# Performance work log

Measured on AMD Instinct MI355X. Metric: run time of the kernel, lower is better.

The kernel has to match this reference:

```python
import jax, jax.numpy as jnp
import numpy as np

N_HEAD = 16

def setup_inputs() -> dict:
    key = jax.random.key(0)
    k1, k2, k3 = jax.random.split(key, 3)
    B, T, C = 2, 2048, 1024
    x = jax.random.normal(k1, (B, T, C), dtype=jnp.float32)
    W_attn = jax.random.normal(k2, (C, 3 * C), dtype=jnp.float32) * (C ** -0.5)
    b_attn = jnp.zeros((3 * C,), dtype=jnp.float32)
    W_proj = jax.random.normal(k3, (C, C), dtype=jnp.float32) * (C ** -0.5)
    b_proj = jnp.zeros((C,), dtype=jnp.float32)
    return {"x": x, "W_attn": W_attn, "b_attn": b_attn, "W_proj": W_proj, "b_proj": b_proj}

def reference(x, W_attn, b_attn, W_proj, b_proj):
    B, T, C = x.shape
    H = N_HEAD
    D = C // H  # head_dim
    scale = D ** -0.5
    qkv = x @ W_attn + b_attn                       # [B,T,3C]
    q, k, v = jnp.split(qkv, 3, axis=-1)
    # [B,T,C] -> [B,H,T,D]
    q = q.reshape(B, T, H, D).transpose(0, 2, 1, 3)
    k = k.reshape(B, T, H, D).transpose(0, 2, 1, 3)
    v = v.reshape(B, T, H, D).transpose(0, 2, 1, 3)
    att = jnp.einsum('bhqd,bhkd->bhqk', q, k) * scale
    causal = jnp.tril(jnp.ones((T, T), dtype=bool))
    att = jnp.where(causal, att, jnp.float32(-jnp.inf))
    att = jax.nn.softmax(att, axis=-1)
    y = jnp.einsum('bhqk,bhkd->bhqd', att, v)       # [B,H,T,D]
    y = y.transpose(0, 2, 1, 3).reshape(B, T, C)
    return y @ W_proj + b_proj
```

## Files before the change

### kernel.cpp

```cpp
#include <hip/hip_runtime.h>

typedef __bf16 bf16;
typedef __bf16 bf16x4 __attribute__((ext_vector_type(4)));
typedef __bf16 bf16x8 __attribute__((ext_vector_type(8)));
typedef short s16x4 __attribute__((ext_vector_type(4)));
typedef float f32x4 __attribute__((ext_vector_type(4)));
typedef unsigned int u32x4 __attribute__((ext_vector_type(4)));

#define NB 2
#define NT 2048
#define NC 1024
#define NH 16
#define ND 64

#if __has_builtin(__builtin_amdgcn_exp2f)
#define EXP2F(x) __builtin_amdgcn_exp2f(x)
#else
#define EXP2F(x) __expf(0.69314718055994531f * (x))
#endif

#if __has_builtin(__builtin_amdgcn_rcpf)
#define RCPF(x) __builtin_amdgcn_rcpf(x)
#else
#define RCPF(x) (1.0f / (x))
#endif

__device__ __forceinline__ void async16(const void* g, void* l) {
  __builtin_amdgcn_global_load_lds(
      (const __attribute__((address_space(1))) void*)g,
      (__attribute__((address_space(3))) void*)l, 16, 0, 0);
}

__device__ __forceinline__ bf16x8 ld8(const bf16* p) {
  return *reinterpret_cast<const bf16x8*>(p);
}
__device__ __forceinline__ bf16x4 ld4(const bf16* p) {
  return *reinterpret_cast<const bf16x4*>(p);
}

__device__ __forceinline__ f32x4 mfma16(bf16x4 a, bf16x4 b, f32x4 c) {
  s16x4 ai = __builtin_bit_cast(s16x4, a);
  s16x4 bi = __builtin_bit_cast(s16x4, b);
#if __has_builtin(__builtin_amdgcn_mfma_f32_16x16x16bf16_1k)
  return __builtin_amdgcn_mfma_f32_16x16x16bf16_1k(ai, bi, c, 0, 0, 0);
#else
  f32x4 d;
  asm("v_mfma_f32_16x16x16_bf16 %0, %1, %2, %3"
      : "=v"(d) : "v"(ai), "v"(bi), "v"(c));
  return d;
#endif
}

__global__ __launch_bounds__(256) void prep(
    const float* __restrict__ x, bf16* __restrict__ xb,
    const float* __restrict__ Wa, bf16* __restrict__ Da,
    const float* __restrict__ Wp, bf16* __restrict__ Dp) {
  int bx = blockIdx.x;
  if (bx < 2048) {
    int i = (bx * 256 + threadIdx.x) * 8;
    const float4* s = (const float4*)(x + i);
    float4 a = s[0], b = s[1];
    bf16x8 o;
    o[0] = (bf16)a.x; o[1] = (bf16)a.y; o[2] = (bf16)a.z; o[3] = (bf16)a.w;
    o[4] = (bf16)b.x; o[5] = (bf16)b.y; o[6] = (bf16)b.z; o[7] = (bf16)b.w;
    *(bf16x8*)(xb + i) = o;
    return;
  }
  __shared__ float tile[32][33];
  int idx = bx - 2048;
  const float* src;
  bf16* dst;
  int Cc, cb, rb;
  if (idx < 96 * 32) { src = Wa; dst = Da; Cc = 3072; cb = idx % 96; rb = idx / 96; }
  else { idx -= 96 * 32; src = Wp; dst = Dp; Cc = 1024; cb = idx % 32; rb = idx / 32; }
  int tx = threadIdx.x & 31, ty = threadIdx.x >> 5;
  int r0 = rb * 32, c0 = cb * 32;
#pragma unroll
  for (int i = 0; i < 4; ++i)
    tile[ty + i * 8][tx] = src[(size_t)(r0 + ty + i * 8) * Cc + c0 + tx];
  __syncthreads();
#pragma unroll
  for (int i = 0; i < 4; ++i)
    dst[(size_t)(c0 + ty + i * 8) * 1024 + r0 + tx] = (bf16)tile[tx][ty + i * 8];
}

__global__ __launch_bounds__(256, 3) void gemm_qkv(
    const bf16* __restrict__ A,
    const bf16* __restrict__ Bt,
    const float* __restrict__ bias,
    bf16* __restrict__ Qo, bf16* __restrict__ Ko, bf16* __restrict__ Vto) {
  const int K = 1024;
  __shared__ bf16 As[128 * 32];
  __shared__ bf16 Bs[128 * 32];
  const int tid = threadIdx.x;
  const int lane = tid & 63, wv = tid >> 6;
  const int quad = lane >> 4, ln = lane & 15;
  const int m0 = blockIdx.x * 128, n0 = blockIdx.y * 128;
  const int wr = (wv >> 1) * 64, wc = (wv & 1) * 64;
  const int rA = tid >> 2, cA = (tid & 3) * 8;
  f32x4 acc[4][4] = {};

  for (int kt = 0; kt < K / 32; ++kt) {
    const int k0 = kt * 32;
#pragma unroll
    for (int inst = 0; inst < 2; ++inst) {
      async16(A + (size_t)(m0 + inst * 64 + rA) * K + k0 + cA,
              &As[inst * 2048 + wv * 512]);
      async16(Bt + (size_t)(n0 + inst * 64 + rA) * K + k0 + cA,
              &Bs[inst * 2048 + wv * 512]);
    }
    __syncthreads();
    bf16x8 aF[4], bF[4];
#pragma unroll
    for (int i = 0; i < 4; ++i) {
      aF[i] = ld8(&As[(wr + i * 16 + ln) * 32 + quad * 8]);
      bF[i] = ld8(&Bs[(wc + i * 16 + ln) * 32 + quad * 8]);
    }
#pragma unroll
    for (int rb = 0; rb < 4; ++rb)
#pragma unroll
      for (int cb = 0; cb < 4; ++cb)
        acc[rb][cb] = __builtin_amdgcn_mfma_f32_16x16x32_bf16(
            aF[rb], bF[cb], acc[rb][cb], 0, 0, 0);
    __syncthreads();
  }
#pragma unroll
  for (int rb = 0; rb < 4; ++rb) {
#pragma unroll
    for (int cb = 0; cb < 4; ++cb) {
      int gn = n0 + wc + cb * 16 + ln;
      int part = gn >> 10, c = gn & 1023;
      int h = c >> 6, dd = c & 63;
      float bs = bias[gn];
      int gm0 = m0 + wr + rb * 16 + quad * 4;
      int b = gm0 >> 11, t0 = gm0 & 2047;
      if (part == 2) {
        bf16x4 vv;
#pragma unroll
        for (int r = 0; r < 4; ++r) vv[r] = (bf16)(acc[rb][cb][r] + bs);
        *(bf16x4*)(Vto + ((size_t)(b * NH + h) * ND + dd) * NT + t0) = vv;
      } else {
        bf16* dst = part == 0 ? Qo : Ko;
        float sc = part == 0 ? 0.18033688f : 1.0f;
#pragma unroll
        for (int r = 0; r < 4; ++r)
          dst[((size_t)(b * NH + h) * NT + t0 + r) * ND + dd] =
              (bf16)((acc[rb][cb][r] + bs) * sc);
      }
    }
  }
}

__global__ __launch_bounds__(512, 4) void flash_attn_kernel(
    const bf16* __restrict__ Qg, const bf16* __restrict__ Kg,
    const bf16* __restrict__ Vtg, bf16* __restrict__ Yg) {
  __shared__ __align__(16) char smem[2][16384];
  const int tid = threadIdx.x;
  const int lane = tid & 63, wv = tid >> 6;
  const int quad = lane >> 4, ln = lane & 15;
  const int bid = blockIdx.x;
  const int qt = 15 - (bid >> 5);
  const int bh = bid & 31;
  const int bb = bh >> 4, hh = bh & 15;
  const int q0w = qt * 128 + wv * 16;
  const bf16* Qp = Qg + ((size_t)bh * NT + q0w) * ND;
  const bf16* Kbase = Kg + (size_t)bh * NT * ND;
  const bf16* Vtbase = Vtg + (size_t)bh * ND * NT;

  const int sub = lane >> 3, sch = lane & 7;
  const int swz = ln & 7;

  bf16x8 qf[2];
#pragma unroll
  for (int ks = 0; ks < 2; ++ks)
    qf[ks] = ld8(Qp + (size_t)ln * ND + ks * 32 + quad * 8);

  f32x4 oacc[4] = {};
  float li = 0.f;

  const int ktiles = 2 * qt + 2;
  const int cw = 2 * qt + 1 + (wv >> 2);

#define STAGE(KT, P)                                                           \
  {                                                                            \
    const int k0s = (KT) * 64;                                                 \
    char* Kl = smem[P];                                                        \
    char* Vl = smem[P] + 8192;                                                 \
    int row = wv * 8 + sub;                                                    \
    int gch = sch ^ sub;                                                       \
    async16(Kbase + (size_t)(k0s + row) * ND + gch * 8, Kl + wv * 8 * 128);    \
    async16(Vtbase + (size_t)row * NT + k0s + gch * 8, Vl + wv * 8 * 128);     \
  }

  STAGE(0, 0);
  for (int kt = 0; kt < ktiles; ++kt) {
    const int p = kt & 1;
    __syncthreads();
    if (kt + 1 < ktiles) STAGE(kt + 1, p ^ 1);
    if (kt < cw) {
      const char* Kl = smem[p];
      const char* Vl = smem[p] + 8192;
      const int k0 = kt * 64;
      f32x4 sacc[4] = {};
#pragma unroll
      for (int ks = 0; ks < 2; ++ks) {
        bf16x8 kfr[4];
#pragma unroll
        for (int cb = 0; cb < 4; ++cb)
          kfr[cb] = *(const bf16x8*)(Kl + (cb * 16 + ln) * 128 +
                                     (((ks * 4 + quad) ^ swz) * 16));
#pragma unroll
        for (int cb = 0; cb < 4; ++cb)
          sacc[cb] = __builtin_amdgcn_mfma_f32_16x16x32_bf16(
              kfr[cb], qf[ks], sacc[cb], 0, 0, 0);
      }
      if (k0 + 63 > q0w) {
        int qr = q0w + ln;
#pragma unroll
        for (int cb = 0; cb < 4; ++cb)
#pragma unroll
          for (int r = 0; r < 4; ++r) {
            int kc = k0 + cb * 16 + quad * 4 + r;
            if (kc > qr) sacc[cb][r] = -1e30f;
          }
      }
      bf16x4 pf[4];
      float rs = 0.f;
#pragma unroll
      for (int cb = 0; cb < 4; ++cb) {
        bf16x4 pv;
#pragma unroll
        for (int r = 0; r < 4; ++r) {
          float pexp = EXP2F(sacc[cb][r]);
          rs += pexp;
          pv[r] = (bf16)pexp;
        }
        pf[cb] = pv;
      }
      li += rs;
#pragma unroll
      for (int cb = 0; cb < 4; ++cb) {
        bf16x4 vfr[4];
#pragma unroll
        for (int db = 0; db < 4; ++db)
          vfr[db] = *(const bf16x4*)(Vl + (db * 16 + ln) * 128 +
                                     (((cb * 2 + (quad >> 1)) ^ swz) * 16) +
                                     (quad & 1) * 8);
#pragma unroll
        for (int db = 0; db < 4; ++db)
          oacc[db] = mfma16(vfr[db], pf[cb], oacc[db]);
      }
    }
  }
#undef STAGE

  li += __shfl_xor(li, 16);
  li += __shfl_xor(li, 32);

  float inv = RCPF(li);
  int row = q0w + ln;
#pragma unroll
  for (int db = 0; db < 4; ++db) {
    bf16x4 ov;
#pragma unroll
    for (int r = 0; r < 4; ++r) ov[r] = (bf16)(oacc[db][r] * inv);
    *(bf16x4*)(Yg + ((size_t)(bb * NT + row)) * NC + hh * 64 + db * 16 +
               quad * 4) = ov;
  }
}

__global__ __launch_bounds__(256, 2) void gemm_proj(
    const bf16* __restrict__ A,
    const bf16* __restrict__ Bt,
    const float* __restrict__ bias,
    float* __restrict__ out) {
  const int K = 1024;
  __shared__ bf16 As[128 * 32];
  __shared__ bf16 Bs[64 * 32];
  const int tid = threadIdx.x;
  const int lane = tid & 63, wv = tid >> 6;
  const int quad = lane >> 4, ln = lane & 15;
  const int m0 = blockIdx.x * 128, n0 = blockIdx.y * 64;
  const int wr = wv * 32;
  const int rA = tid >> 2, cA = (tid & 3) * 8;
  f32x4 acc[2][4] = {};

  for (int kt = 0; kt < K / 32; ++kt) {
    const int k0 = kt * 32;
#pragma unroll
    for (int inst = 0; inst < 2; ++inst)
      async16(A + (size_t)(m0 + inst * 64 + rA) * K + k0 + cA,
              &As[inst * 2048 + wv * 512]);
    async16(Bt + (size_t)(n0 + rA) * K + k0 + cA, &Bs[wv * 512]);
    __syncthreads();
    bf16x8 aF[2], bF[4];
#pragma unroll
    for (int i = 0; i < 2; ++i)
      aF[i] = ld8(&As[(wr + i * 16 + ln) * 32 + quad * 8]);
#pragma unroll
    for (int i = 0; i < 4; ++i)
      bF[i] = ld8(&Bs[(i * 16 + ln) * 32 + quad * 8]);
#pragma unroll
    for (int rb = 0; rb < 2; ++rb)
#pragma unroll
      for (int cb = 0; cb < 4; ++cb)
        acc[rb][cb] = __builtin_amdgcn_mfma_f32_16x16x32_bf16(
            aF[rb], bF[cb], acc[rb][cb], 0, 0, 0);
    __syncthreads();
  }
#pragma unroll
  for (int rb = 0; rb < 2; ++rb) {
#pragma unroll
    for (int cb = 0; cb < 4; ++cb) {
      int gn = n0 + cb * 16 + ln;
      float bs = bias[gn];
#pragma unroll
      for (int r = 0; r < 4; ++r) {
        int gm = m0 + wr + rb * 16 + quad * 4 + r;
        out[(size_t)gm * 1024 + gn] = acc[rb][cb][r] + bs;
      }
    }
  }
}

extern "C" void kernel_launch(void* const* d_in, const int* in_sizes, int n_in,
                              void* d_out, int out_size, void* d_ws, size_t ws_size,
                              hipStream_t stream) {
  const float* x      = (const float*)d_in[0];
  const float* W_attn = (const float*)d_in[1];
  const float* b_attn = (const float*)d_in[2];
  const float* W_proj = (const float*)d_in[3];
  const float* b_proj = (const float*)d_in[4];
  float* out = (float*)d_out;

  bf16* ws  = (bf16*)d_ws;
  bf16* xb  = ws;
  bf16* Wab = xb + (size_t)4096 * 1024;
  bf16* Wpb = Wab + (size_t)3072 * 1024;
  bf16* Qb  = Wpb + (size_t)1024 * 1024;
  bf16* Kb  = Qb + (size_t)32 * 2048 * 64;
  bf16* Vtb = Kb + (size_t)32 * 2048 * 64;
  bf16* Yb  = xb;

  prep<<<2048 + 96 * 32 + 32 * 32, 256, 0, stream>>>(x, xb, W_attn, Wab,
                                                     W_proj, Wpb);
  gemm_qkv<<<dim3(32, 24), 256, 0, stream>>>(xb, Wab, b_attn, Qb, Kb, Vtb);
  flash_attn_kernel<<<512, 512, 0, stream>>>(Qb, Kb, Vtb, Yb);
  gemm_proj<<<dim3(32, 16), 256, 0, stream>>>(Yb, Wpb, b_proj, out);
}
```

Before: 170.4 us.

## Give each attention wave two 16-row query blocks to reuse K/V fragments

The flash attention kernel now runs 4 waves of 256 threads per block instead of 8, and each wave handles 32 query rows (two 16-row sub-blocks) instead of 16. Each K and V fragment read from shared memory feeds twice as many MFMAs, cutting LDS read traffic per FLOP, and each thread issues two async loads per tensor per stage. In exchange, per-wave register pressure roughly doubles for the accumulators, and fewer waves per block may reduce latency hiding. The launch bound also changes to (256,3).

```diff
diff --git a/kernel.cpp b/kernel.cpp
--- a/kernel.cpp
+++ b/kernel.cpp
@@ -151,7 +151,7 @@
   }
 }
 
-__global__ __launch_bounds__(512, 4) void flash_attn_kernel(
+__global__ __launch_bounds__(256, 3) void flash_attn_kernel(
     const bf16* __restrict__ Qg, const bf16* __restrict__ Kg,
     const bf16* __restrict__ Vtg, bf16* __restrict__ Yg) {
   __shared__ __align__(16) char smem[2][16384];
@@ -162,7 +162,7 @@
   const int qt = 15 - (bid >> 5);
   const int bh = bid & 31;
   const int bb = bh >> 4, hh = bh & 15;
-  const int q0w = qt * 128 + wv * 16;
+  const int q0w = qt * 128 + wv * 32;
   const bf16* Qp = Qg + ((size_t)bh * NT + q0w) * ND;
   const bf16* Kbase = Kg + (size_t)bh * NT * ND;
   const bf16* Vtbase = Vtg + (size_t)bh * ND * NT;
@@ -170,26 +170,32 @@
   const int sub = lane >> 3, sch = lane & 7;
   const int swz = ln & 7;
 
-  bf16x8 qf[2];
-#pragma unroll
-  for (int ks = 0; ks < 2; ++ks)
-    qf[ks] = ld8(Qp + (size_t)ln * ND + ks * 32 + quad * 8);
-
-  f32x4 oacc[4] = {};
-  float li = 0.f;
+  bf16x8 qf[2][2];
+#pragma unroll
+  for (int qb = 0; qb < 2; ++qb)
+#pragma unroll
+    for (int ks = 0; ks < 2; ++ks)
+      qf[qb][ks] = ld8(Qp + (size_t)(qb * 16 + ln) * ND + ks * 32 + quad * 8);
+
+  f32x4 oacc[2][4] = {};
+  float li[2] = {0.f, 0.f};
 
   const int ktiles = 2 * qt + 2;
-  const int cw = 2 * qt + 1 + (wv >> 2);
+  const int cw = 2 * qt + 1 + (wv >> 1);
 
 #define STAGE(KT, P)                                                           \
   {                                                                            \
     const int k0s = (KT) * 64;                                                 \
     char* Kl = smem[P];                                                        \
     char* Vl = smem[P] + 8192;                                                 \
-    int row = wv * 8 + sub;                                                    \
+    int r0s = wv * 16 + sub;                                                   \
     int gch = sch ^ sub;                                                       \
-    async16(Kbase + (size_t)(k0s + row) * ND + gch * 8, Kl + wv * 8 * 128);    \
-    async16(Vtbase + (size_t)row * NT + k0s + gch * 8, Vl + wv * 8 * 128);     \
+    async16(Kbase + (size_t)(k0s + r0s) * ND + gch * 8, Kl + wv * 16 * 128);   \
+    async16(Kbase + (size_t)(k0s + r0s + 8) * ND + gch * 8,                    \
+            Kl + wv * 16 * 128 + 1024);                                        \
+    async16(Vtbase + (size_t)r0s * NT + k0s + gch * 8, Vl + wv * 16 * 128);    \
+    async16(Vtbase + (size_t)(r0s + 8) * NT + k0s + gch * 8,                   \
+            Vl + wv * 16 * 128 + 1024);                                        \
   }
 
   STAGE(0, 0);
@@ -201,7 +207,7 @@
       const char* Kl = smem[p];
       const char* Vl = smem[p] + 8192;
       const int k0 = kt * 64;
-      f32x4 sacc[4] = {};
+      f32x4 sacc[2][4] = {};
 #pragma unroll
       for (int ks = 0; ks < 2; ++ks) {
         bf16x8 kfr[4];
@@ -210,34 +216,42 @@
           kfr[cb] = *(const bf16x8*)(Kl + (cb * 16 + ln) * 128 +
                                      (((ks * 4 + quad) ^ swz) * 16));
 #pragma unroll
-        for (int cb = 0; cb < 4; ++cb)
-          sacc[cb] = __builtin_amdgcn_mfma_f32_16x16x32_bf16(
-              kfr[cb], qf[ks], sacc[cb], 0, 0, 0);
+        for (int qb = 0; qb < 2; ++qb)
+#pragma unroll
+          for (int cb = 0; cb < 4; ++cb)
+            sacc[qb][cb] = __builtin_amdgcn_mfma_f32_16x16x32_bf16(
+                kfr[cb], qf[qb][ks], sacc[qb][cb], 0, 0, 0);
       }
       if (k0 + 63 > q0w) {
-        int qr = q0w + ln;
-#pragma unroll
-        for (int cb = 0; cb < 4; ++cb)
+#pragma unroll
+        for (int qb = 0; qb < 2; ++qb) {
+          int qr = q0w + qb * 16 + ln;
+#pragma unroll
+          for (int cb = 0; cb < 4; ++cb)
+#pragma unroll
+            for (int r = 0; r < 4; ++r) {
+              int kc = k0 + cb * 16 + quad * 4 + r;
+              if (kc > qr) sacc[qb][cb][r] = -1e30f;
+            }
+        }
+      }
+      bf16x4 pf[2][4];
+#pragma unroll
+      for (int qb = 0; qb < 2; ++qb) {
+        float rs = 0.f;
+#pragma unroll
+        for (int cb = 0; cb < 4; ++cb) {
+          bf16x4 pv;
 #pragma unroll
           for (int r = 0; r < 4; ++r) {
-            int kc = k0 + cb * 16 + quad * 4 + r;
-            if (kc > qr) sacc[cb][r] = -1e30f;
+            float pexp = EXP2F(sacc[qb][cb][r]);
+            rs += pexp;
+            pv[r] = (bf16)pexp;
           }
-      }
-      bf16x4 pf[4];
-      float rs = 0.f;
-#pragma unroll
-      for (int cb = 0; cb < 4; ++cb) {
-        bf16x4 pv;
-#pragma unroll
-        for (int r = 0; r < 4; ++r) {
-          float pexp = EXP2F(sacc[cb][r]);
-          rs += pexp;
-          pv[r] = (bf16)pexp;
+          pf[qb][cb] = pv;
         }
-        pf[cb] = pv;
-      }
-      li += rs;
+        li[qb] += rs;
+      }
 #pragma unroll
       for (int cb = 0; cb < 4; ++cb) {
         bf16x4 vfr[4];
@@ -247,25 +261,30 @@
                                      (((cb * 2 + (quad >> 1)) ^ swz) * 16) +
                                      (quad & 1) * 8);
 #pragma unroll
-        for (int db = 0; db < 4; ++db)
-          oacc[db] = mfma16(vfr[db], pf[cb], oacc[db]);
+        for (int qb = 0; qb < 2; ++qb)
+#pragma unroll
+          for (int db = 0; db < 4; ++db)
+            oacc[qb][db] = mfma16(vfr[db], pf[qb][cb], oacc[qb][db]);
       }
     }
   }
 #undef STAGE
 
-  li += __shfl_xor(li, 16);
-  li += __shfl_xor(li, 32);
-
-  float inv = RCPF(li);
-  int row = q0w + ln;
-#pragma unroll
-  for (int db = 0; db < 4; ++db) {
-    bf16x4 ov;
-#pragma unroll
-    for (int r = 0; r < 4; ++r) ov[r] = (bf16)(oacc[db][r] * inv);
-    *(bf16x4*)(Yg + ((size_t)(bb * NT + row)) * NC + hh * 64 + db * 16 +
-               quad * 4) = ov;
+#pragma unroll
+  for (int qb = 0; qb < 2; ++qb) {
+    float l = li[qb];
+    l += __shfl_xor(l, 16);
+    l += __shfl_xor(l, 32);
+    float inv = RCPF(l);
+    int row = q0w + qb * 16 + ln;
+#pragma unroll
+    for (int db = 0; db < 4; ++db) {
+      bf16x4 ov;
+#pragma unroll
+      for (int r = 0; r < 4; ++r) ov[r] = (bf16)(oacc[qb][db][r] * inv);
+      *(bf16x4*)(Yg + ((size_t)(bb * NT + row)) * NC + hh * 64 + db * 16 +
+                 quad * 4) = ov;
+    }
   }
 }
 
@@ -345,6 +364,6 @@
   prep<<<2048 + 96 * 32 + 32 * 32, 256, 0, stream>>>(x, xb, W_attn, Wab,
                                                      W_proj, Wpb);
   gemm_qkv<<<dim3(32, 24), 256, 0, stream>>>(xb, Wab, b_attn, Qb, Kb, Vtb);
-  flash_attn_kernel<<<512, 512, 0, stream>>>(Qb, Kb, Vtb, Yb);
+  flash_attn_kernel<<<512, 256, 0, stream>>>(Qb, Kb, Vtb, Yb);
   gemm_proj<<<dim3(32, 16), 256, 0, stream>>>(Yb, Wpb, b_proj, out);
 }
```

After: 167.8 us. About the same (-1.5%).
